# Kernel optimization log

Hardware: AMD Instinct MI355X
Metric: run time of the kernel (lower is better)

Reference implementation:

```python
import jax, jax.numpy as jnp
import numpy as np

B, Q, PAST = 2, 1024, 1024
T = Q + PAST
HID, NH, NKV, HD = 4096, 32, 8, 128
MAXPOS = 4096
SCALE = HD ** -0.5


def setup_inputs() -> dict:
    key = jax.random.key(0)
    ks = jax.random.split(key, 8)
    hidden_states = jax.random.normal(ks[0], (B, Q, HID), jnp.float32)
    attention_mask = jnp.ones((B, T), jnp.int32)  # all tokens valid
    position_ids = jnp.broadcast_to(
        jnp.arange(PAST, PAST + Q, dtype=jnp.int64)[None, :], (B, Q))
    # standard RoPE caches: [max_pos, head_dim/2]
    inv = 1.0 / (10000.0 ** (np.arange(0, HD, 2, dtype=np.float64) / HD))
    ang = np.arange(MAXPOS, dtype=np.float64)[:, None] * inv[None, :]
    rope_cos_freqs = jnp.asarray(np.cos(ang), jnp.float32)
    rope_sin_freqs = jnp.asarray(np.sin(ang), jnp.float32)
    past_key = jax.random.normal(ks[1], (B, NKV, PAST, HD), jnp.float32)
    past_value = jax.random.normal(ks[2], (B, NKV, PAST, HD), jnp.float32)
    q_w = jax.random.normal(ks[3], (NH * HD, HID), jnp.float32) * 0.02
    k_w = jax.random.normal(ks[4], (NKV * HD, HID), jnp.float32) * 0.02
    v_w = jax.random.normal(ks[5], (NKV * HD, HID), jnp.float32) * 0.02
    o_w = jax.random.normal(ks[6], (HID, NH * HD), jnp.float32) * 0.02
    return {"hidden_states": hidden_states, "attention_mask": attention_mask,
            "position_ids": position_ids, "rope_cos_freqs": rope_cos_freqs,
            "rope_sin_freqs": rope_sin_freqs, "past_key": past_key,
            "past_value": past_value, "q_w": q_w, "k_w": k_w, "v_w": v_w,
            "o_w": o_w}


def _rope(x, cos, sin):
    # x: [B,S,n_heads,HD]; cos/sin: [B,S,HD/2]; non-interleaved (half split)
    d2 = x.shape[-1] // 2
    x1, x2 = x[..., :d2], x[..., d2:]
    c, s = cos[:, :, None, :], sin[:, :, None, :]
    return jnp.concatenate([x1 * c - x2 * s, x2 * c + x1 * s], axis=-1)


def reference(hidden_states, attention_mask, position_ids, rope_cos_freqs,
              rope_sin_freqs, past_key, past_value, q_w, k_w, v_w, o_w):
    b, q_len, _ = hidden_states.shape
    q = jnp.einsum('bsh,oh->bso', hidden_states, q_w).reshape(b, q_len, NH, HD)
    k = jnp.einsum('bsh,oh->bso', hidden_states, k_w).reshape(b, q_len, NKV, HD)
    v = jnp.einsum('bsh,oh->bso', hidden_states, v_w).reshape(b, q_len, NKV, HD)

    cos = rope_cos_freqs[position_ids]  # [B,Q,HD/2]
    sin = rope_sin_freqs[position_ids]
    q = _rope(q, cos, sin)
    k = _rope(k, cos, sin)

    # append to KV cache -> [B,NKV,T,HD]
    present_key = jnp.concatenate([past_key, k.transpose(0, 2, 1, 3)], axis=2)
    present_value = jnp.concatenate([past_value, v.transpose(0, 2, 1, 3)], axis=2)

    # additive causal + padding mask built from cumsum of attention_mask
    all_idx = jnp.cumsum(attention_mask, axis=-1)            # [B,T]
    full = (all_idx[:, -q_len:, None] >= all_idx[:, None, :]) \
        & attention_mask[:, None, :].astype(bool)            # [B,Q,T]
    bias = jnp.where(full, 0.0, -10000.0)[:, None, :, :]     # [B,1,Q,T]

    group = NH // NKV
    k_rep = jnp.repeat(present_key, group, axis=1)           # [B,NH,T,HD]
    v_rep = jnp.repeat(present_value, group, axis=1)

    scores = jnp.einsum('bqhd,bhkd->bhqk', q, k_rep) * SCALE + bias
    probs = jax.nn.softmax(scores, axis=-1)
    ctx = jnp.einsum('bhqk,bhkd->bqhd', probs, v_rep).reshape(b, q_len, NH * HD)
    attn_out = jnp.einsum('bso,ho->bsh', ctx, o_w)
    return attn_out, present_key, present_value
```

## Files before the change

### kernel.cpp

```cpp
#include <hip/hip_runtime.h>
#include <hip/hip_bf16.h>
#include <stdint.h>

typedef __bf16 bf16_t;
typedef bf16_t bf16x8 __attribute__((ext_vector_type(8)));
typedef bf16_t bf16x4 __attribute__((ext_vector_type(4)));
typedef float f32x4 __attribute__((ext_vector_type(4)));

#define B_ 2
#define Q_ 1024
#define PAST_ 1024
#define T_ 2048
#define HID_ 4096
#define NH_ 32
#define NKV_ 8
#define HD_ 128
#define SCALE_ 0.08838834764831845f

__device__ __forceinline__ void async_cp16(const bf16_t* g, bf16_t* l) {
  __builtin_amdgcn_global_load_lds((__attribute__((address_space(1))) void*)g,
                                   (__attribute__((address_space(3))) void*)l, 16, 0, 0);
}

__global__ void cvt_f32_bf16(const float* __restrict__ src, bf16_t* __restrict__ dst, size_t n) {
  size_t i = ((size_t)blockIdx.x * blockDim.x + threadIdx.x) * 8;
  if (i >= n) return;
  float4 a = *(const float4*)(src + i);
  float4 b = *(const float4*)(src + i + 4);
  bf16x8 o;
  o[0] = (bf16_t)a.x; o[1] = (bf16_t)a.y; o[2] = (bf16_t)a.z; o[3] = (bf16_t)a.w;
  o[4] = (bf16_t)b.x; o[5] = (bf16_t)b.y; o[6] = (bf16_t)b.z; o[7] = (bf16_t)b.w;
  *(bf16x8*)(dst + i) = o;
}

__global__ void copy_past(const float* __restrict__ pk, const float* __restrict__ pv,
                          float* __restrict__ oK, float* __restrict__ oV,
                          bf16_t* __restrict__ Kall) {
  size_t i = ((size_t)blockIdx.x * 256 + threadIdx.x) * 4;
  if (i >= (size_t)B_ * NKV_ * PAST_ * HD_) return;
  int d = (int)(i & 127);
  size_t r = i >> 7;
  int t = (int)(r & 1023); r >>= 10;
  int g = (int)(r & 7); int b = (int)(r >> 3);
  size_t dst = (((size_t)b * NKV_ + g) * T_ + t) * HD_ + d;
  float4 k4 = *(const float4*)(pk + i);
  float4 v4 = *(const float4*)(pv + i);
  *(float4*)(oK + dst) = k4;
  *(float4*)(oV + dst) = v4;
  bf16x4 kb; kb[0] = (bf16_t)k4.x; kb[1] = (bf16_t)k4.y; kb[2] = (bf16_t)k4.z; kb[3] = (bf16_t)k4.w;
  *(bf16x4*)(Kall + dst) = kb;
}

__global__ void build_vt(const float* __restrict__ past_v, const float* __restrict__ QKV,
                         bf16_t* __restrict__ Vt) {
  __shared__ bf16_t tile[64][136];
  const int tid = threadIdx.x;
  const int t0 = blockIdx.x * 64, g = blockIdx.y, b = blockIdx.z;
#pragma unroll
  for (int k = 0; k < 8; ++k) {
    int idx = k * 256 + tid;
    int t = idx >> 5, dc = (idx & 31) * 4;
    int tt = t0 + t;
    const float* src = (tt < PAST_)
        ? past_v + ((((size_t)b * NKV_ + g) * PAST_ + tt) * HD_ + dc)
        : QKV + (((size_t)b * Q_ + (tt - PAST_)) * 6144 + 5120 + g * HD_ + dc);
    float4 v4 = *(const float4*)src;
    tile[t][dc] = (bf16_t)v4.x; tile[t][dc + 1] = (bf16_t)v4.y;
    tile[t][dc + 2] = (bf16_t)v4.z; tile[t][dc + 3] = (bf16_t)v4.w;
  }
  __syncthreads();
#pragma unroll
  for (int k = 0; k < 4; ++k) {
    int idx = k * 256 + tid;
    int d = idx >> 3, c = idx & 7;
    bf16x8 o;
#pragma unroll
    for (int j = 0; j < 8; ++j) o[j] = tile[c * 8 + j][d];
    *(bf16x8*)(Vt + ((((size_t)b * NKV_ + g) * HD_ + d) * T_) + t0 + c * 8) = o;
  }
}

__device__ __forceinline__ void stage_tile(const bf16_t* __restrict__ G, int ldg,
                                           bf16_t* __restrict__ L, int tid) {
#pragma unroll
  for (int t = 0; t < 4; ++t) {
    int c = t * 512 + tid;
    int row = c >> 3, sc = (c & 7) ^ (row & 7);
    int cb = t * 512 + (tid & 448);
    async_cp16(G + (size_t)row * ldg + sc * 8, L + (size_t)cb * 8);
  }
}

__device__ __forceinline__ void stage_tileA128(const bf16_t* __restrict__ G, int ldg,
                                               bf16_t* __restrict__ L, int tid) {
#pragma unroll
  for (int t = 0; t < 2; ++t) {
    int c = t * 512 + tid;
    int row = c >> 3, sc = (c & 7) ^ (row & 7);
    int cb = t * 512 + (tid & 448);
    async_cp16(G + (size_t)row * ldg + sc * 8, L + (size_t)cb * 8);
  }
}

__global__ __launch_bounds__(512, 2)
void gemm256(const bf16_t* __restrict__ A, const bf16_t* __restrict__ W,
             float* __restrict__ C, int M, int N, int K) {
  __shared__ bf16_t sm[2][2][16384];
  const int tid = threadIdx.x;
  const int lane = tid & 63;
  const int quad = lane >> 4, l15 = lane & 15;
  const int wave = tid >> 6;
  const int wm = wave >> 2, wn = wave & 3;
  const int bm = blockIdx.y * 256, bn = blockIdx.x * 256;
  const int NT = K >> 6;

  const bf16_t* Ag = A + (size_t)bm * K;
  const bf16_t* Wg = W + (size_t)bn * K;

  f32x4 acc[8][4] = {};

  stage_tile(Ag, K, &sm[0][0][0], tid);
  stage_tile(Wg, K, &sm[0][1][0], tid);
  stage_tile(Ag + 64, K, &sm[1][0][0], tid);
  stage_tile(Wg + 64, K, &sm[1][1][0], tid);
  asm volatile("s_waitcnt vmcnt(8)" ::: "memory");
  __builtin_amdgcn_s_barrier();

  const int arow = wm * 128 + l15;
  const int brow = wn * 64 + l15;
  const int pq = l15 & 7;

  for (int t = 0; t < NT; ++t) {
    const bf16_t* lA = &sm[t & 1][0][0];
    const bf16_t* lB = &sm[t & 1][1][0];
    const int k2 = (t + 2) << 6;
    bf16x8 af[4][2], bf01[2][2], bf23[2][2];

#pragma unroll
    for (int m = 0; m < 4; ++m)
#pragma unroll
      for (int kk = 0; kk < 2; ++kk)
        af[m][kk] = *(const bf16x8*)(lA + (arow + m * 16) * 64 + ((((kk << 2) + quad) ^ pq) << 3));
#pragma unroll
    for (int n = 0; n < 2; ++n)
#pragma unroll
      for (int kk = 0; kk < 2; ++kk)
        bf01[n][kk] = *(const bf16x8*)(lB + (brow + n * 16) * 64 + ((((kk << 2) + quad) ^ pq) << 3));
    __builtin_amdgcn_s_barrier();
    asm volatile("s_waitcnt lgkmcnt(0)" ::: "memory");
    __builtin_amdgcn_sched_barrier(0);
    __builtin_amdgcn_s_setprio(1);
#pragma unroll
    for (int m = 0; m < 4; ++m)
#pragma unroll
      for (int n = 0; n < 2; ++n)
#pragma unroll
        for (int kk = 0; kk < 2; ++kk)
          acc[m][n] = __builtin_amdgcn_mfma_f32_16x16x32_bf16(af[m][kk], bf01[n][kk], acc[m][n], 0, 0, 0);
    __builtin_amdgcn_s_setprio(0);
    __builtin_amdgcn_s_barrier();

#pragma unroll
    for (int n = 0; n < 2; ++n)
#pragma unroll
      for (int kk = 0; kk < 2; ++kk)
        bf23[n][kk] = *(const bf16x8*)(lB + (brow + (n + 2) * 16) * 64 + ((((kk << 2) + quad) ^ pq) << 3));
    __builtin_amdgcn_s_barrier();
    asm volatile("s_waitcnt lgkmcnt(0)" ::: "memory");
    __builtin_amdgcn_sched_barrier(0);
    __builtin_amdgcn_s_setprio(1);
#pragma unroll
    for (int m = 0; m < 4; ++m)
#pragma unroll
      for (int n = 0; n < 2; ++n)
#pragma unroll
        for (int kk = 0; kk < 2; ++kk)
          acc[m][n + 2] = __builtin_amdgcn_mfma_f32_16x16x32_bf16(af[m][kk], bf23[n][kk], acc[m][n + 2], 0, 0, 0);
    __builtin_amdgcn_s_setprio(0);
    __builtin_amdgcn_s_barrier();

#pragma unroll
    for (int m = 0; m < 4; ++m)
#pragma unroll
      for (int kk = 0; kk < 2; ++kk)
        af[m][kk] = *(const bf16x8*)(lA + (arow + (m + 4) * 16) * 64 + ((((kk << 2) + quad) ^ pq) << 3));
    if (t + 2 < NT) stage_tile(Wg + k2, K, &sm[t & 1][1][0], tid);
    __builtin_amdgcn_s_barrier();
    asm volatile("s_waitcnt lgkmcnt(0)" ::: "memory");
    __builtin_amdgcn_sched_barrier(0);
    __builtin_amdgcn_s_setprio(1);
#pragma unroll
    for (int m = 0; m < 4; ++m)
#pragma unroll
      for (int n = 0; n < 2; ++n)
#pragma unroll
        for (int kk = 0; kk < 2; ++kk)
          acc[m + 4][n + 2] = __builtin_amdgcn_mfma_f32_16x16x32_bf16(af[m][kk], bf23[n][kk], acc[m + 4][n + 2], 0, 0, 0);
    __builtin_amdgcn_s_setprio(0);
    __builtin_amdgcn_s_barrier();

    if (t + 2 < NT) stage_tile(Ag + k2, K, &sm[t & 1][0][0], tid);
    __builtin_amdgcn_s_barrier();
    __builtin_amdgcn_s_setprio(1);
#pragma unroll
    for (int m = 0; m < 4; ++m)
#pragma unroll
      for (int n = 0; n < 2; ++n)
#pragma unroll
        for (int kk = 0; kk < 2; ++kk)
          acc[m + 4][n] = __builtin_amdgcn_mfma_f32_16x16x32_bf16(af[m][kk], bf01[n][kk], acc[m + 4][n], 0, 0, 0);
    __builtin_amdgcn_s_setprio(0);
    if (t + 2 < NT)
      asm volatile("s_waitcnt vmcnt(8)" ::: "memory");
    else if (t + 2 == NT)
      asm volatile("s_waitcnt vmcnt(0)" ::: "memory");
    __builtin_amdgcn_s_barrier();
  }

#pragma unroll
  for (int m = 0; m < 8; ++m) {
    int row0 = bm + wm * 128 + m * 16 + quad * 4;
#pragma unroll
    for (int n = 0; n < 4; ++n) {
      int col = bn + wn * 64 + n * 16 + l15;
#pragma unroll
      for (int r = 0; r < 4; ++r)
        C[(size_t)(row0 + r) * N + col] = acc[m][n][r];
    }
  }
}

__global__ __launch_bounds__(512, 2)
void gemm128(const bf16_t* __restrict__ A, const bf16_t* __restrict__ W,
             float* __restrict__ C, int M, int N, int K) {
  __shared__ bf16_t smA[2][8192];
  __shared__ bf16_t smB[2][16384];
  const int tid = threadIdx.x;
  const int lane = tid & 63;
  const int quad = lane >> 4, l15 = lane & 15;
  const int wave = tid >> 6;
  const int wm = wave >> 2, wn = wave & 3;
  const int bm = blockIdx.y * 128, bn = blockIdx.x * 256;
  const int NT = K >> 6;

  const bf16_t* Ag = A + (size_t)bm * K;
  const bf16_t* Wg = W + (size_t)bn * K;

  f32x4 acc[4][4] = {};

  stage_tileA128(Ag, K, &smA[0][0], tid);
  stage_tile(Wg, K, &smB[0][0], tid);
  stage_tileA128(Ag + 64, K, &smA[1][0], tid);
  stage_tile(Wg + 64, K, &smB[1][0], tid);
  asm volatile("s_waitcnt vmcnt(6)" ::: "memory");
  __builtin_amdgcn_s_barrier();

  const int arow = wm * 64 + l15;
  const int brow = wn * 64 + l15;
  const int pq = l15 & 7;

  for (int t = 0; t < NT; ++t) {
    const bf16_t* lA = &smA[t & 1][0];
    const bf16_t* lB = &smB[t & 1][0];
    const int k2 = (t + 2) << 6;
    bf16x8 af[2][2], bf01[2][2], bf23[2][2];

#pragma unroll
    for (int m = 0; m < 2; ++m)
#pragma unroll
      for (int kk = 0; kk < 2; ++kk)
        af[m][kk] = *(const bf16x8*)(lA + (arow + m * 16) * 64 + ((((kk << 2) + quad) ^ pq) << 3));
#pragma unroll
    for (int n = 0; n < 2; ++n)
#pragma unroll
      for (int kk = 0; kk < 2; ++kk)
        bf01[n][kk] = *(const bf16x8*)(lB + (brow + n * 16) * 64 + ((((kk << 2) + quad) ^ pq) << 3));
    __builtin_amdgcn_s_barrier();
    asm volatile("s_waitcnt lgkmcnt(0)" ::: "memory");
    __builtin_amdgcn_sched_barrier(0);
    __builtin_amdgcn_s_setprio(1);
#pragma unroll
    for (int m = 0; m < 2; ++m)
#pragma unroll
      for (int n = 0; n < 2; ++n)
#pragma unroll
        for (int kk = 0; kk < 2; ++kk)
          acc[m][n] = __builtin_amdgcn_mfma_f32_16x16x32_bf16(af[m][kk], bf01[n][kk], acc[m][n], 0, 0, 0);
    __builtin_amdgcn_s_setprio(0);
    __builtin_amdgcn_s_barrier();

#pragma unroll
    for (int n = 0; n < 2; ++n)
#pragma unroll
      for (int kk = 0; kk < 2; ++kk)
        bf23[n][kk] = *(const bf16x8*)(lB + (brow + (n + 2) * 16) * 64 + ((((kk << 2) + quad) ^ pq) << 3));
    __builtin_amdgcn_s_barrier();
    asm volatile("s_waitcnt lgkmcnt(0)" ::: "memory");
    __builtin_amdgcn_sched_barrier(0);
    __builtin_amdgcn_s_setprio(1);
#pragma unroll
    for (int m = 0; m < 2; ++m)
#pragma unroll
      for (int n = 0; n < 2; ++n)
#pragma unroll
        for (int kk = 0; kk < 2; ++kk)
          acc[m][n + 2] = __builtin_amdgcn_mfma_f32_16x16x32_bf16(af[m][kk], bf23[n][kk], acc[m][n + 2], 0, 0, 0);
    __builtin_amdgcn_s_setprio(0);
    __builtin_amdgcn_s_barrier();

#pragma unroll
    for (int m = 0; m < 2; ++m)
#pragma unroll
      for (int kk = 0; kk < 2; ++kk)
        af[m][kk] = *(const bf16x8*)(lA + (arow + (m + 2) * 16) * 64 + ((((kk << 2) + quad) ^ pq) << 3));
    if (t + 2 < NT) stage_tile(Wg + k2, K, &smB[t & 1][0], tid);
    __builtin_amdgcn_s_barrier();
    asm volatile("s_waitcnt lgkmcnt(0)" ::: "memory");
    __builtin_amdgcn_sched_barrier(0);
    __builtin_amdgcn_s_setprio(1);
#pragma unroll
    for (int m = 0; m < 2; ++m)
#pragma unroll
      for (int n = 0; n < 2; ++n)
#pragma unroll
        for (int kk = 0; kk < 2; ++kk)
          acc[m + 2][n + 2] = __builtin_amdgcn_mfma_f32_16x16x32_bf16(af[m][kk], bf23[n][kk], acc[m + 2][n + 2], 0, 0, 0);
    __builtin_amdgcn_s_setprio(0);
    __builtin_amdgcn_s_barrier();

    if (t + 2 < NT) stage_tileA128(Ag + k2, K, &smA[t & 1][0], tid);
    __builtin_amdgcn_s_barrier();
    __builtin_amdgcn_s_setprio(1);
#pragma unroll
    for (int m = 0; m < 2; ++m)
#pragma unroll
      for (int n = 0; n < 2; ++n)
#pragma unroll
        for (int kk = 0; kk < 2; ++kk)
          acc[m + 2][n] = __builtin_amdgcn_mfma_f32_16x16x32_bf16(af[m][kk], bf01[n][kk], acc[m + 2][n], 0, 0, 0);
    __builtin_amdgcn_s_setprio(0);
    if (t + 2 < NT)
      asm volatile("s_waitcnt vmcnt(6)" ::: "memory");
    else if (t + 2 == NT)
      asm volatile("s_waitcnt vmcnt(0)" ::: "memory");
    __builtin_amdgcn_s_barrier();
  }

#pragma unroll
  for (int m = 0; m < 4; ++m) {
    int row0 = bm + wm * 64 + m * 16 + quad * 4;
#pragma unroll
    for (int n = 0; n < 4; ++n) {
      int col = bn + wn * 64 + n * 16 + l15;
#pragma unroll
      for (int r = 0; r < 4; ++r)
        C[(size_t)(row0 + r) * N + col] = acc[m][n][r];
    }
  }
}

__global__ void rope_scatter(const float* __restrict__ QKV, const float* __restrict__ cosf,
                             const float* __restrict__ sinf, const int* __restrict__ pos_ids,
                             bf16_t* __restrict__ Qr, bf16_t* __restrict__ Kall,
                             float* __restrict__ outK, float* __restrict__ outV) {
  int m = blockIdx.x;
  int b = m >> 10, s = m & 1023;
  int pos = pos_ids[(size_t)b * Q_ + s];
  const float* row = QKV + (size_t)m * 6144;
  int tid = threadIdx.x;
  for (int p = tid; p < NH_ * 64; p += 256) {
    int h = p >> 6, d = p & 63;
    float x1 = row[h * 128 + d], x2 = row[h * 128 + d + 64];
    float c = cosf[pos * 64 + d], sn = sinf[pos * 64 + d];
    size_t qb = (((size_t)b * NH_ + h) * Q_ + s) * HD_;
    Qr[qb + d] = (bf16_t)((x1 * c - x2 * sn) * SCALE_);
    Qr[qb + d + 64] = (bf16_t)((x2 * c + x1 * sn) * SCALE_);
  }
  for (int p = tid; p < NKV_ * 64; p += 256) {
    int g = p >> 6, d = p & 63;
    float x1 = row[4096 + g * 128 + d], x2 = row[4096 + g * 128 + d + 64];
    float c = cosf[pos * 64 + d], sn = sinf[pos * 64 + d];
    float o1 = x1 * c - x2 * sn, o2 = x2 * c + x1 * sn;
    size_t kbi = (((size_t)b * NKV_ + g) * T_ + PAST_ + s) * HD_;
    Kall[kbi + d] = (bf16_t)o1; Kall[kbi + d + 64] = (bf16_t)o2;
    outK[kbi + d] = o1; outK[kbi + d + 64] = o2;
  }
  for (int e = tid; e < NKV_ * HD_; e += 256) {
    int g = e >> 7, d = e & 127;
    float v = row[5120 + g * 128 + d];
    outV[(((size_t)b * NKV_ + g) * T_ + PAST_ + s) * HD_ + d] = v;
  }
}

__global__ __launch_bounds__(512, 2)
void attn_fwd(const bf16_t* __restrict__ Qr, const bf16_t* __restrict__ Kall,
              const bf16_t* __restrict__ Vt, bf16_t* __restrict__ Ctx) {
  __shared__ bf16_t lK[2][64 * 128];
  __shared__ bf16_t lV[2][128 * 64];
  __shared__ bf16_t lP[8 * 2 * 16 * 64];
  const int tid = threadIdx.x;
  const int wave = tid >> 6, lane = tid & 63;
  const int quad = lane >> 4, l15 = lane & 15;
  const int i = blockIdx.x;
  const int xcd = i & 7;
  const int j = i >> 3;
  const int pairsel = j & 1;
  const int idx = j >> 1;
  const int h_in = idx & 3;
  const int qt = 3 - (idx >> 2);
  const int b = pairsel, kv = xcd;
  const int h = kv * 4 + h_in;
  const int qbase = qt * 256;
  const int wq = qbase + wave * 32;
  const size_t kvbase = ((size_t)b * NKV_ + kv) * T_ * HD_;
  const size_t vtbase = ((size_t)b * NKV_ + kv) * HD_ * T_;

  auto stageKV = [&](int kb, int s) {
#pragma unroll
    for (int t = 0; t < 2; ++t) {
      int c = t * 512 + tid;
      int row = c >> 4, sc = (c & 15) ^ (row & 15);
      int cb = t * 512 + (tid & 448);
      async_cp16(Kall + kvbase + (size_t)(kb + row) * HD_ + sc * 8, lK[s] + (size_t)cb * 8);
    }
#pragma unroll
    for (int t = 0; t < 2; ++t) {
      int c = t * 512 + tid;
      int d = c >> 3, sc = (c & 7) ^ (d & 7);
      int cb = t * 512 + (tid & 448);
      async_cp16(Vt + vtbase + (size_t)d * T_ + kb + sc * 8, lV[s] + (size_t)cb * 8);
    }
  };

  bf16x8 qf[2][4];
#pragma unroll
  for (int g = 0; g < 2; ++g) {
    const bf16_t* qg = Qr + ((((size_t)b * NH_ + h) * Q_) + wq + g * 16 + l15) * HD_ + quad * 8;
#pragma unroll
    for (int kk = 0; kk < 4; ++kk) qf[g][kk] = *(const bf16x8*)(qg + kk * 32);
  }
  bf16x8 ones;
#pragma unroll
  for (int e = 0; e < 8; ++e) ones[e] = (bf16_t)1.0f;

  f32x4 ctx[2][8] = {};
  float Mr[2][4], Lr[2][4];
#pragma unroll
  for (int g = 0; g < 2; ++g)
#pragma unroll
    for (int r = 0; r < 4; ++r) { Mr[g][r] = -3.0e30f; Lr[g][r] = 0.0f; }
  bf16_t* lPw0 = lP + wave * 2048;
  bf16_t* lPw1 = lPw0 + 1024;
  const int nt = (PAST_ + qbase + 256) >> 6;

  stageKV(0, 0);

  for (int ti = 0; ti < nt; ++ti) {
    const int kb = ti << 6;
    const int cur = ti & 1;
    if (ti + 1 < nt) {
      stageKV(kb + 64, cur ^ 1);
      asm volatile("s_waitcnt vmcnt(4)" ::: "memory");
    } else {
      asm volatile("s_waitcnt vmcnt(0)" ::: "memory");
    }
    __builtin_amdgcn_s_barrier();
    asm volatile("" ::: "memory");
    if (kb <= PAST_ + wq + 31) {
      const bf16_t* cK = lK[cur];
      const bf16_t* cV = lV[cur];
      f32x4 sacc[2][4];
#pragma unroll
      for (int g = 0; g < 2; ++g)
#pragma unroll
        for (int nc = 0; nc < 4; ++nc) sacc[g][nc] = (f32x4){0.f, 0.f, 0.f, 0.f};
      __builtin_amdgcn_s_setprio(1);
#pragma unroll
      for (int nc = 0; nc < 4; ++nc) {
        bf16x8 bk[4];
#pragma unroll
        for (int kk = 0; kk < 4; ++kk)
          bk[kk] = *(const bf16x8*)(cK + (nc * 16 + l15) * 128 + (((kk * 4 + quad) ^ l15) << 3));
#pragma unroll
        for (int kk = 0; kk < 4; ++kk)
          sacc[0][nc] = __builtin_amdgcn_mfma_f32_16x16x32_bf16(qf[0][kk], bk[kk], sacc[0][nc], 0, 0, 0);
#pragma unroll
        for (int kk = 0; kk < 4; ++kk)
          sacc[1][nc] = __builtin_amdgcn_mfma_f32_16x16x32_bf16(qf[1][kk], bk[kk], sacc[1][nc], 0, 0, 0);
      }
      __builtin_amdgcn_s_setprio(0);
      bool need = false;
      float tmax[2][4];
#pragma unroll
      for (int g = 0; g < 2; ++g) {
        int wqg = wq + g * 16;
        bool fullvis = (kb + 63 <= PAST_ + wqg);
        if (!fullvis) {
#pragma unroll
          for (int nc = 0; nc < 4; ++nc) {
            int tkey = kb + nc * 16 + l15;
#pragma unroll
            for (int r = 0; r < 4; ++r)
              if (tkey > PAST_ + wqg + quad * 4 + r) sacc[g][nc][r] -= 10000.0f;
          }
        }
#pragma unroll
        for (int r = 0; r < 4; ++r) {
          float tm = fmaxf(fmaxf(sacc[g][0][r], sacc[g][1][r]), fmaxf(sacc[g][2][r], sacc[g][3][r]));
#pragma unroll
          for (int mmk = 1; mmk < 16; mmk <<= 1) tm = fmaxf(tm, __shfl_xor(tm, mmk, 64));
          tmax[g][r] = tm;
          need = need || (tm > Mr[g][r] + 8.0f);
        }
      }
      if (__any(need)) {
#pragma unroll
        for (int g = 0; g < 2; ++g)
#pragma unroll
          for (int r = 0; r < 4; ++r) {
            float nm = fmaxf(Mr[g][r], tmax[g][r]);
            float al = __expf(Mr[g][r] - nm);
            Mr[g][r] = nm;
            Lr[g][r] *= al;
#pragma unroll
            for (int nc2 = 0; nc2 < 8; ++nc2) ctx[g][nc2][r] *= al;
          }
      }
#pragma unroll
      for (int g = 0; g < 2; ++g) {
        bf16_t* lPw = g ? lPw1 : lPw0;
#pragma unroll
        for (int nc = 0; nc < 4; ++nc)
#pragma unroll
          for (int r = 0; r < 4; ++r) {
            float p = __expf(sacc[g][nc][r] - Mr[g][r]);
            int rho = quad * 4 + r;
            int cslot = ((nc * 2 + (l15 >> 3)) ^ (rho & 7));
            lPw[rho * 64 + cslot * 8 + (l15 & 7)] = (bf16_t)p;
          }
      }
      asm volatile("s_waitcnt lgkmcnt(0)" ::: "memory");
      __builtin_amdgcn_sched_barrier(0);
      bf16x8 ap0[2], ap1[2];
#pragma unroll
      for (int kk2 = 0; kk2 < 2; ++kk2) {
        int off = (((kk2 * 4 + quad) ^ (l15 & 7)) << 3);
        ap0[kk2] = *(const bf16x8*)(lPw0 + l15 * 64 + off);
        ap1[kk2] = *(const bf16x8*)(lPw1 + l15 * 64 + off);
      }
      __builtin_amdgcn_s_setprio(1);
      f32x4 ls0 = (f32x4){0.f, 0.f, 0.f, 0.f}, ls1 = (f32x4){0.f, 0.f, 0.f, 0.f};
#pragma unroll
      for (int kk2 = 0; kk2 < 2; ++kk2) {
        ls0 = __builtin_amdgcn_mfma_f32_16x16x32_bf16(ap0[kk2], ones, ls0, 0, 0, 0);
        ls1 = __builtin_amdgcn_mfma_f32_16x16x32_bf16(ap1[kk2], ones, ls1, 0, 0, 0);
      }
#pragma unroll
      for (int nc2 = 0; nc2 < 8; ++nc2)
#pragma unroll
        for (int kk2 = 0; kk2 < 2; ++kk2) {
          bf16x8 bv = *(const bf16x8*)(cV + (nc2 * 16 + l15) * 64 + (((kk2 * 4 + quad) ^ (l15 & 7)) << 3));
          ctx[0][nc2] = __builtin_amdgcn_mfma_f32_16x16x32_bf16(ap0[kk2], bv, ctx[0][nc2], 0, 0, 0);
          ctx[1][nc2] = __builtin_amdgcn_mfma_f32_16x16x32_bf16(ap1[kk2], bv, ctx[1][nc2], 0, 0, 0);
        }
      __builtin_amdgcn_s_setprio(0);
#pragma unroll
      for (int r = 0; r < 4; ++r) { Lr[0][r] += ls0[r]; Lr[1][r] += ls1[r]; }
    }
    __builtin_amdgcn_sched_barrier(0);
    __builtin_amdgcn_s_barrier();
  }
#pragma unroll
  for (int g = 0; g < 2; ++g) {
    float inv[4];
#pragma unroll
    for (int r = 0; r < 4; ++r) inv[r] = 1.0f / Lr[g][r];
#pragma unroll
    for (int nc2 = 0; nc2 < 8; ++nc2)
#pragma unroll
      for (int r = 0; r < 4; ++r) {
        size_t row = (size_t)b * Q_ + wq + g * 16 + quad * 4 + r;
        Ctx[row * (NH_ * HD_) + h * HD_ + nc2 * 16 + l15] = (bf16_t)(ctx[g][nc2][r] * inv[r]);
      }
  }
}

extern "C" void kernel_launch(void* const* d_in, const int* in_sizes, int n_in,
                              void* d_out, int out_size, void* d_ws, size_t ws_size,
                              hipStream_t stream) {
  const float* hidden = (const float*)d_in[0];
  const int* pos = (const int*)d_in[2];
  const float* cosf = (const float*)d_in[3];
  const float* sinf = (const float*)d_in[4];
  const float* past_k = (const float*)d_in[5];
  const float* past_v = (const float*)d_in[6];
  const float* q_w = (const float*)d_in[7];
  const float* k_w = (const float*)d_in[8];
  const float* v_w = (const float*)d_in[9];
  const float* o_w = (const float*)d_in[10];

  float* attn_out = (float*)d_out;
  float* outK = attn_out + (size_t)B_ * Q_ * HID_;
  float* outV = outK + (size_t)B_ * NKV_ * T_ * HD_;

  if (ws_size < 150994944) return;
  char* ws = (char*)d_ws;
  bf16_t* Wqkv = (bf16_t*)(ws);
  bf16_t* Xb   = (bf16_t*)(ws + 50331648);
  float*  QKV  = (float*)(ws + 67108864);
  bf16_t* Qr   = (bf16_t*)(ws + 117440512);
  bf16_t* Kall = (bf16_t*)(ws + 134217728);
  bf16_t* Vt   = (bf16_t*)(ws + 142606336);
  bf16_t* Wo   = (bf16_t*)(ws + 67108864);
  bf16_t* Ctx  = (bf16_t*)(ws + 50331648);

  cvt_f32_bf16<<<4096, 256, 0, stream>>>(hidden, Xb, 8388608);
  cvt_f32_bf16<<<8192, 256, 0, stream>>>(q_w, Wqkv, 16777216);
  cvt_f32_bf16<<<2048, 256, 0, stream>>>(k_w, Wqkv + 16777216, 4194304);
  cvt_f32_bf16<<<2048, 256, 0, stream>>>(v_w, Wqkv + 20971520, 4194304);
  copy_past<<<2048, 256, 0, stream>>>(past_k, past_v, outK, outV, Kall);
  gemm256<<<dim3(24, 8), 512, 0, stream>>>(Xb, Wqkv, QKV, 2048, 6144, 4096);
  rope_scatter<<<2048, 256, 0, stream>>>(QKV, cosf, sinf, pos, Qr, Kall, outK, outV);
  build_vt<<<dim3(32, 8, 2), 256, 0, stream>>>(past_v, QKV, Vt);
  cvt_f32_bf16<<<8192, 256, 0, stream>>>(o_w, Wo, 16777216);
  attn_fwd<<<256, 512, 0, stream>>>(Qr, Kall, Vt, Ctx);
  gemm128<<<dim3(16, 16), 512, 0, stream>>>(Ctx, Wo, attn_out, 2048, 4096, 4096);
}
```

Baseline: 568.2 us.

## Use 256x192 QKV GEMM tiles and fold past-V transpose into copy_past

```diff
diff --git a/kernel.cpp b/kernel.cpp
--- a/kernel.cpp
+++ b/kernel.cpp
@@ -35,36 +35,24 @@
 
 __global__ void copy_past(const float* __restrict__ pk, const float* __restrict__ pv,
                           float* __restrict__ oK, float* __restrict__ oV,
-                          bf16_t* __restrict__ Kall) {
-  size_t i = ((size_t)blockIdx.x * 256 + threadIdx.x) * 4;
-  if (i >= (size_t)B_ * NKV_ * PAST_ * HD_) return;
-  int d = (int)(i & 127);
-  size_t r = i >> 7;
-  int t = (int)(r & 1023); r >>= 10;
-  int g = (int)(r & 7); int b = (int)(r >> 3);
-  size_t dst = (((size_t)b * NKV_ + g) * T_ + t) * HD_ + d;
-  float4 k4 = *(const float4*)(pk + i);
-  float4 v4 = *(const float4*)(pv + i);
-  *(float4*)(oK + dst) = k4;
-  *(float4*)(oV + dst) = v4;
-  bf16x4 kb; kb[0] = (bf16_t)k4.x; kb[1] = (bf16_t)k4.y; kb[2] = (bf16_t)k4.z; kb[3] = (bf16_t)k4.w;
-  *(bf16x4*)(Kall + dst) = kb;
-}
-
-__global__ void build_vt(const float* __restrict__ past_v, const float* __restrict__ QKV,
-                         bf16_t* __restrict__ Vt) {
+                          bf16_t* __restrict__ Kall, bf16_t* __restrict__ Vt) {
   __shared__ bf16_t tile[64][136];
   const int tid = threadIdx.x;
   const int t0 = blockIdx.x * 64, g = blockIdx.y, b = blockIdx.z;
+  const size_t srcbase = (((size_t)b * NKV_ + g) * PAST_ + t0) * HD_;
+  const size_t dstbase = (((size_t)b * NKV_ + g) * T_ + t0) * HD_;
 #pragma unroll
   for (int k = 0; k < 8; ++k) {
     int idx = k * 256 + tid;
     int t = idx >> 5, dc = (idx & 31) * 4;
-    int tt = t0 + t;
-    const float* src = (tt < PAST_)
-        ? past_v + ((((size_t)b * NKV_ + g) * PAST_ + tt) * HD_ + dc)
-        : QKV + (((size_t)b * Q_ + (tt - PAST_)) * 6144 + 5120 + g * HD_ + dc);
-    float4 v4 = *(const float4*)src;
+    size_t so = srcbase + (size_t)t * HD_ + dc;
+    size_t dofs = dstbase + (size_t)t * HD_ + dc;
+    float4 k4 = *(const float4*)(pk + so);
+    float4 v4 = *(const float4*)(pv + so);
+    *(float4*)(oK + dofs) = k4;
+    *(float4*)(oV + dofs) = v4;
+    bf16x4 kb; kb[0] = (bf16_t)k4.x; kb[1] = (bf16_t)k4.y; kb[2] = (bf16_t)k4.z; kb[3] = (bf16_t)k4.w;
+    *(bf16x4*)(Kall + dofs) = kb;
     tile[t][dc] = (bf16_t)v4.x; tile[t][dc + 1] = (bf16_t)v4.y;
     tile[t][dc + 2] = (bf16_t)v4.z; tile[t][dc + 3] = (bf16_t)v4.w;
   }
@@ -80,8 +68,34 @@
   }
 }
 
-__device__ __forceinline__ void stage_tile(const bf16_t* __restrict__ G, int ldg,
-                                           bf16_t* __restrict__ L, int tid) {
+__global__ void build_vt(const float* __restrict__ QKV, bf16_t* __restrict__ Vt) {
+  __shared__ bf16_t tile[64][136];
+  const int tid = threadIdx.x;
+  const int t0 = PAST_ + blockIdx.x * 64, g = blockIdx.y, b = blockIdx.z;
+#pragma unroll
+  for (int k = 0; k < 8; ++k) {
+    int idx = k * 256 + tid;
+    int t = idx >> 5, dc = (idx & 31) * 4;
+    int s = t0 - PAST_ + t;
+    const float* src = QKV + (((size_t)b * Q_ + s) * 6144 + 5120 + g * HD_ + dc);
+    float4 v4 = *(const float4*)src;
+    tile[t][dc] = (bf16_t)v4.x; tile[t][dc + 1] = (bf16_t)v4.y;
+    tile[t][dc + 2] = (bf16_t)v4.z; tile[t][dc + 3] = (bf16_t)v4.w;
+  }
+  __syncthreads();
+#pragma unroll
+  for (int k = 0; k < 4; ++k) {
+    int idx = k * 256 + tid;
+    int d = idx >> 3, c = idx & 7;
+    bf16x8 o;
+#pragma unroll
+    for (int j = 0; j < 8; ++j) o[j] = tile[c * 8 + j][d];
+    *(bf16x8*)(Vt + ((((size_t)b * NKV_ + g) * HD_ + d) * T_) + t0 + c * 8) = o;
+  }
+}
+
+__device__ __forceinline__ void stage_tile256(const bf16_t* __restrict__ G, int ldg,
+                                              bf16_t* __restrict__ L, int tid) {
 #pragma unroll
   for (int t = 0; t < 4; ++t) {
     int c = t * 512 + tid;
@@ -91,8 +105,19 @@
   }
 }
 
-__device__ __forceinline__ void stage_tileA128(const bf16_t* __restrict__ G, int ldg,
-                                               bf16_t* __restrict__ L, int tid) {
+__device__ __forceinline__ void stage_tile192(const bf16_t* __restrict__ G, int ldg,
+                                              bf16_t* __restrict__ L, int tid) {
+#pragma unroll
+  for (int t = 0; t < 3; ++t) {
+    int c = t * 512 + tid;
+    int row = c >> 3, sc = (c & 7) ^ (row & 7);
+    int cb = t * 512 + (tid & 448);
+    async_cp16(G + (size_t)row * ldg + sc * 8, L + (size_t)cb * 8);
+  }
+}
+
+__device__ __forceinline__ void stage_tile128(const bf16_t* __restrict__ G, int ldg,
+                                              bf16_t* __restrict__ L, int tid) {
 #pragma unroll
   for (int t = 0; t < 2; ++t) {
     int c = t * 512 + tid;
@@ -103,38 +128,39 @@
 }
 
 __global__ __launch_bounds__(512, 2)
-void gemm256(const bf16_t* __restrict__ A, const bf16_t* __restrict__ W,
+void gemm192(const bf16_t* __restrict__ A, const bf16_t* __restrict__ W,
              float* __restrict__ C, int M, int N, int K) {
-  __shared__ bf16_t sm[2][2][16384];
+  __shared__ bf16_t smA[2][16384];
+  __shared__ bf16_t smB[2][12288];
   const int tid = threadIdx.x;
   const int lane = tid & 63;
   const int quad = lane >> 4, l15 = lane & 15;
   const int wave = tid >> 6;
   const int wm = wave >> 2, wn = wave & 3;
-  const int bm = blockIdx.y * 256, bn = blockIdx.x * 256;
+  const int bm = blockIdx.y * 256, bn = blockIdx.x * 192;
   const int NT = K >> 6;
 
   const bf16_t* Ag = A + (size_t)bm * K;
   const bf16_t* Wg = W + (size_t)bn * K;
 
-  f32x4 acc[8][4] = {};
-
-  stage_tile(Ag, K, &sm[0][0][0], tid);
-  stage_tile(Wg, K, &sm[0][1][0], tid);
-  stage_tile(Ag + 64, K, &sm[1][0][0], tid);
-  stage_tile(Wg + 64, K, &sm[1][1][0], tid);
-  asm volatile("s_waitcnt vmcnt(8)" ::: "memory");
+  f32x4 acc[8][3] = {};
+
+  stage_tile256(Ag, K, &smA[0][0], tid);
+  stage_tile192(Wg, K, &smB[0][0], tid);
+  stage_tile256(Ag + 64, K, &smA[1][0], tid);
+  stage_tile192(Wg + 64, K, &smB[1][0], tid);
+  asm volatile("s_waitcnt vmcnt(7)" ::: "memory");
   __builtin_amdgcn_s_barrier();
 
   const int arow = wm * 128 + l15;
-  const int brow = wn * 64 + l15;
+  const int brow = wn * 48 + l15;
   const int pq = l15 & 7;
 
   for (int t = 0; t < NT; ++t) {
-    const bf16_t* lA = &sm[t & 1][0][0];
-    const bf16_t* lB = &sm[t & 1][1][0];
+    const bf16_t* lA = &smA[t & 1][0];
+    const bf16_t* lB = &smB[t & 1][0];
     const int k2 = (t + 2) << 6;
-    bf16x8 af[4][2], bf01[2][2], bf23[2][2];
+    bf16x8 af[4][2], bf01[2][2], bf2[2];
 
 #pragma unroll
     for (int m = 0; m < 4; ++m)
@@ -161,10 +187,8 @@
     __builtin_amdgcn_s_barrier();
 
 #pragma unroll
-    for (int n = 0; n < 2; ++n)
-#pragma unroll
-      for (int kk = 0; kk < 2; ++kk)
-        bf23[n][kk] = *(const bf16x8*)(lB + (brow + (n + 2) * 16) * 64 + ((((kk << 2) + quad) ^ pq) << 3));
+    for (int kk = 0; kk < 2; ++kk)
+      bf2[kk] = *(const bf16x8*)(lB + (brow + 32) * 64 + ((((kk << 2) + quad) ^ pq) << 3));
     __builtin_amdgcn_s_barrier();
     asm volatile("s_waitcnt lgkmcnt(0)" ::: "memory");
     __builtin_amdgcn_sched_barrier(0);
@@ -172,10 +196,8 @@
 #pragma unroll
     for (int m = 0; m < 4; ++m)
 #pragma unroll
-      for (int n = 0; n < 2; ++n)
-#pragma unroll
-        for (int kk = 0; kk < 2; ++kk)
-          acc[m][n + 2] = __builtin_amdgcn_mfma_f32_16x16x32_bf16(af[m][kk], bf23[n][kk], acc[m][n + 2], 0, 0, 0);
+      for (int kk = 0; kk < 2; ++kk)
+        acc[m][2] = __builtin_amdgcn_mfma_f32_16x16x32_bf16(af[m][kk], bf2[kk], acc[m][2], 0, 0, 0);
     __builtin_amdgcn_s_setprio(0);
     __builtin_amdgcn_s_barrier();
 
@@ -184,7 +206,7 @@
 #pragma unroll
       for (int kk = 0; kk < 2; ++kk)
         af[m][kk] = *(const bf16x8*)(lA + (arow + (m + 4) * 16) * 64 + ((((kk << 2) + quad) ^ pq) << 3));
-    if (t + 2 < NT) stage_tile(Wg + k2, K, &sm[t & 1][1][0], tid);
+    if (t + 2 < NT) stage_tile192(Wg + k2, K, &smB[t & 1][0], tid);
     __builtin_amdgcn_s_barrier();
     asm volatile("s_waitcnt lgkmcnt(0)" ::: "memory");
     __builtin_amdgcn_sched_barrier(0);
@@ -192,14 +214,12 @@
 #pragma unroll
     for (int m = 0; m < 4; ++m)
 #pragma unroll
-      for (int n = 0; n < 2; ++n)
-#pragma unroll
-        for (int kk = 0; kk < 2; ++kk)
-          acc[m + 4][n + 2] = __builtin_amdgcn_mfma_f32_16x16x32_bf16(af[m][kk], bf23[n][kk], acc[m + 4][n + 2], 0, 0, 0);
-    __builtin_amdgcn_s_setprio(0);
-    __builtin_amdgcn_s_barrier();
-
-    if (t + 2 < NT) stage_tile(Ag + k2, K, &sm[t & 1][0][0], tid);
+      for (int kk = 0; kk < 2; ++kk)
+        acc[m + 4][2] = __builtin_amdgcn_mfma_f32_16x16x32_bf16(af[m][kk], bf2[kk], acc[m + 4][2], 0, 0, 0);
+    __builtin_amdgcn_s_setprio(0);
+    __builtin_amdgcn_s_barrier();
+
+    if (t + 2 < NT) stage_tile256(Ag + k2, K, &smA[t & 1][0], tid);
     __builtin_amdgcn_s_barrier();
     __builtin_amdgcn_s_setprio(1);
 #pragma unroll
@@ -211,7 +231,7 @@
           acc[m + 4][n] = __builtin_amdgcn_mfma_f32_16x16x32_bf16(af[m][kk], bf01[n][kk], acc[m + 4][n], 0, 0, 0);
     __builtin_amdgcn_s_setprio(0);
     if (t + 2 < NT)
-      asm volatile("s_waitcnt vmcnt(8)" ::: "memory");
+      asm volatile("s_waitcnt vmcnt(7)" ::: "memory");
     else if (t + 2 == NT)
       asm volatile("s_waitcnt vmcnt(0)" ::: "memory");
     __builtin_amdgcn_s_barrier();
@@ -221,8 +241,8 @@
   for (int m = 0; m < 8; ++m) {
     int row0 = bm + wm * 128 + m * 16 + quad * 4;
 #pragma unroll
-    for (int n = 0; n < 4; ++n) {
-      int col = bn + wn * 64 + n * 16 + l15;
+    for (int n = 0; n < 3; ++n) {
+      int col = bn + wn * 48 + n * 16 + l15;
 #pragma unroll
       for (int r = 0; r < 4; ++r)
         C[(size_t)(row0 + r) * N + col] = acc[m][n][r];
@@ -248,10 +268,10 @@
 
   f32x4 acc[4][4] = {};
 
-  stage_tileA128(Ag, K, &smA[0][0], tid);
-  stage_tile(Wg, K, &smB[0][0], tid);
-  stage_tileA128(Ag + 64, K, &smA[1][0], tid);
-  stage_tile(Wg + 64, K, &smB[1][0], tid);
+  stage_tile128(Ag, K, &smA[0][0], tid);
+  stage_tile256(Wg, K, &smB[0][0], tid);
+  stage_tile128(Ag + 64, K, &smA[1][0], tid);
+  stage_tile256(Wg + 64, K, &smB[1][0], tid);
   asm volatile("s_waitcnt vmcnt(6)" ::: "memory");
   __builtin_amdgcn_s_barrier();
 
@@ -313,7 +333,7 @@
 #pragma unroll
       for (int kk = 0; kk < 2; ++kk)
         af[m][kk] = *(const bf16x8*)(lA + (arow + (m + 2) * 16) * 64 + ((((kk << 2) + quad) ^ pq) << 3));
-    if (t + 2 < NT) stage_tile(Wg + k2, K, &smB[t & 1][0], tid);
+    if (t + 2 < NT) stage_tile256(Wg + k2, K, &smB[t & 1][0], tid);
     __builtin_amdgcn_s_barrier();
     asm volatile("s_waitcnt lgkmcnt(0)" ::: "memory");
     __builtin_amdgcn_sched_barrier(0);
@@ -328,7 +348,7 @@
     __builtin_amdgcn_s_setprio(0);
     __builtin_amdgcn_s_barrier();
 
-    if (t + 2 < NT) stage_tileA128(Ag + k2, K, &smA[t & 1][0], tid);
+    if (t + 2 < NT) stage_tile128(Ag + k2, K, &smA[t & 1][0], tid);
     __builtin_amdgcn_s_barrier();
     __builtin_amdgcn_s_setprio(1);
 #pragma unroll
@@ -618,10 +638,10 @@
   cvt_f32_bf16<<<8192, 256, 0, stream>>>(q_w, Wqkv, 16777216);
   cvt_f32_bf16<<<2048, 256, 0, stream>>>(k_w, Wqkv + 16777216, 4194304);
   cvt_f32_bf16<<<2048, 256, 0, stream>>>(v_w, Wqkv + 20971520, 4194304);
-  copy_past<<<2048, 256, 0, stream>>>(past_k, past_v, outK, outV, Kall);
-  gemm256<<<dim3(24, 8), 512, 0, stream>>>(Xb, Wqkv, QKV, 2048, 6144, 4096);
+  copy_past<<<dim3(16, 8, 2), 256, 0, stream>>>(past_k, past_v, outK, outV, Kall, Vt);
+  gemm192<<<dim3(32, 8), 512, 0, stream>>>(Xb, Wqkv, QKV, 2048, 6144, 4096);
   rope_scatter<<<2048, 256, 0, stream>>>(QKV, cosf, sinf, pos, Qr, Kall, outK, outV);
-  build_vt<<<dim3(32, 8, 2), 256, 0, stream>>>(past_v, QKV, Vt);
+  build_vt<<<dim3(16, 8, 2), 256, 0, stream>>>(QKV, Vt);
   cvt_f32_bf16<<<8192, 256, 0, stream>>>(o_w, Wo, 16777216);
   attn_fwd<<<256, 512, 0, stream>>>(Qr, Kall, Vt, Ctx);
   gemm128<<<dim3(16, 16), 512, 0, stream>>>(Ctx, Wo, attn_out, 2048, 4096, 4096);
```

Measured after the change: 551.7 us. -2.9%, faster.
